# Kernel optimization log

Hardware: AMD Instinct MI355X
Metric: run time of the kernel (lower is better)

Reference implementation:

```python
import jax, jax.numpy as jnp
import numpy as np

B, N, IN_F, E, H, A = 8, 1024, 1024, 256, 4, 64
ALPHA = 0.2          # leaky relu slope
NEG = -9e15          # mask value from original code


def setup_inputs() -> dict:
    key = jax.random.key(0)
    k = jax.random.split(key, 7)
    x = jax.random.normal(k[0], (B * N, IN_F), dtype=jnp.float32)
    adj = jax.random.randint(k[1], (B, N, N), 0, 2, dtype=jnp.int32)
    # per-head GAT params: W (H, IN_F, E); a split into a1, a2 (H, E) each,
    # since cat([Wh_i, Wh_j]) @ a == Wh_i @ a1 + Wh_j @ a2 exactly.
    W = jax.random.normal(k[2], (H, IN_F, E), dtype=jnp.float32) * 0.05
    a1 = jax.random.normal(k[3], (H, E), dtype=jnp.float32) * 0.05
    a2 = jax.random.normal(k[4], (H, E), dtype=jnp.float32) * 0.05
    W_act = jax.random.normal(k[5], (H * E, A), dtype=jnp.float32) * 0.05
    b_act = jnp.zeros((A,), dtype=jnp.float32)
    return {"x": x, "adj": adj, "W": W, "a1": a1, "a2": a2,
            "W_act": W_act, "b_act": b_act}


def reference(x, adj, W, a1, a2, W_act, b_act):
    b, n, _ = adj.shape
    xr = x.reshape(b, n, -1)                                   # (B, N, IN_F)
    Wh = jnp.einsum('bni,hio->hbno', xr, W)                    # (H, B, N, E)
    f1 = jnp.einsum('hbno,ho->hbn', Wh, a1)                    # a . Wh_i part
    f2 = jnp.einsum('hbno,ho->hbn', Wh, a2)                    # a . Wh_j part
    e = jax.nn.leaky_relu(f1[..., :, None] + f2[..., None, :], ALPHA)  # (H,B,N,N)
    e = jnp.where(adj[None] > 0, e, NEG)
    att = jax.nn.softmax(e, axis=-1)                           # masked softmax
    h_prime = jnp.einsum('hbnm,hbmo->hbno', att, Wh)           # (H, B, N, E)
    h_prime = jax.nn.elu(h_prime)                              # concat=True -> elu
    feat = jnp.transpose(h_prime, (1, 2, 0, 3)).reshape(b * n, H * E)
    return feat @ W_act + b_act                                # (B*N, A)
```

## Files before the change

kernel.cpp:

```cpp
#include <hip/hip_runtime.h>
#include <stdint.h>

typedef __attribute__((ext_vector_type(8))) short short8;
typedef __attribute__((ext_vector_type(4))) float f32x4;
typedef __attribute__((ext_vector_type(16))) float f32x16;


__device__ __forceinline__ float b2f(unsigned short u) {
    union { unsigned int i; float f; } v; v.i = ((unsigned int)u) << 16; return v.f;
}
__device__ __forceinline__ unsigned short f2b(float f) {
    union { float f; unsigned int i; } v; v.f = f;
    unsigned int u = v.i;
    u = (u + 0x7FFFu + ((u >> 16) & 1u)) >> 16;
    return (unsigned short)u;
}
__device__ __forceinline__ void glds16(const void* g, const void* l) {
    __builtin_amdgcn_global_load_lds(
        (const __attribute__((address_space(1))) unsigned int*)g,
        (__attribute__((address_space(3))) unsigned int*)l, 16, 0, 0);
}

__device__ __forceinline__ void cvt8(const void* in, unsigned short* out,
                                     int f, int grp) {
    if (f) {
        ((ushort4*)out)[grp * 2]     = ((const ushort4*)in)[grp * 2];
        ((ushort4*)out)[grp * 2 + 1] = ((const ushort4*)in)[grp * 2 + 1];
    } else {
        const float4* p = (const float4*)in + (size_t)grp * 2;
        float4 a = p[0], b = p[1];
        ushort4 o0, o1;
        o0.x = f2b(a.x); o0.y = f2b(a.y); o0.z = f2b(a.z); o0.w = f2b(a.w);
        o1.x = f2b(b.x); o1.y = f2b(b.y); o1.z = f2b(b.z); o1.w = f2b(b.w);
        ((ushort4*)out)[grp * 2]     = o0;
        ((ushort4*)out)[grp * 2 + 1] = o1;
    }
}

__global__ void prep_small(const unsigned int* __restrict__ x,
                           const void* __restrict__ a1, const void* __restrict__ a2,
                           const void* __restrict__ bact,
                           unsigned short* __restrict__ a1b,
                           unsigned short* __restrict__ a2b,
                           unsigned short* __restrict__ bactb,
                           int* __restrict__ flag) {
    __shared__ int sflag;
    int tid = threadIdx.x;
    if (tid < 64) {
        unsigned int wv = x[tid];
        unsigned int e = (wv >> 7) & 0xFF;
        unsigned long long m = __ballot(e >= 100 && e <= 140);
        if (tid == 0) { sflag = (__popcll(m) >= 48) ? 1 : 0; flag[0] = sflag; }
    }
    __syncthreads();
    int f = sflag;
    if (tid < 128) cvt8(a1, a1b, f, tid);
    else           cvt8(a2, a2b, f, tid - 128);
    if (tid < 8)   cvt8(bact, bactb, f, tid);
}

__global__ void conv8(const void* __restrict__ in, unsigned short* __restrict__ out,
                      const int* __restrict__ flag, int total8) {
    int i = blockIdx.x * 256 + threadIdx.x;
    if (i >= total8) return;
    cvt8(in, out, *flag, i);
}

__global__ void zero_kern(float4* __restrict__ p) {
    p[blockIdx.x * 256 + threadIdx.x] = float4{0.f, 0.f, 0.f, 0.f};
}

__global__ __launch_bounds__(256) void t2_all(
        const void* __restrict__ Win, const void* __restrict__ Wactin,
        unsigned short* __restrict__ WT, unsigned short* __restrict__ WactT,
        const int* __restrict__ flag) {
    __shared__ unsigned int tile[64 * 65];
    int z = blockIdx.z;
    const void* in; unsigned short* out; int C, bt;
    if (z < 4) { in = Win; out = WT; C = 256; bt = z; }
    else { if (blockIdx.x != 0) return; in = Wactin; out = WactT; C = 64; bt = 0; }
    int t = threadIdx.x;
    int c0 = blockIdx.x * 64;
    int r0 = blockIdx.y * 64;
    int rl = t >> 2;
    int cc = (t & 3) * 16;
    size_t ibase = ((size_t)bt * 1024 + (r0 + rl)) * C + c0 + cc;
    unsigned short v[16];
    if (*flag) {
        const unsigned short* p = (const unsigned short*)in + ibase;
        short8 a = *(const short8*)p;
        short8 b = *(const short8*)(p + 8);
#pragma unroll
        for (int j = 0; j < 8; j++) { v[j] = (unsigned short)a[j]; v[8 + j] = (unsigned short)b[j]; }
    } else {
        const float* p = (const float*)in + ibase;
#pragma unroll
        for (int j = 0; j < 16; j++) v[j] = f2b(p[j]);
    }
#pragma unroll
    for (int j = 0; j < 16; j++)
        tile[(cc + j) * 65 + rl] = v[j];
    __syncthreads();
    int cl = t >> 2;
    int rch = (t & 3) * 16;
    unsigned short o[16];
#pragma unroll
    for (int j = 0; j < 16; j++)
        o[j] = (unsigned short)tile[cl * 65 + rch + j];
    unsigned short* op = out + ((size_t)bt * C + (c0 + cl)) * 1024 + r0 + rch;
#pragma unroll
    for (int q = 0; q < 4; q++) {
        ushort4 s; s.x = o[q*4]; s.y = o[q*4+1]; s.z = o[q*4+2]; s.w = o[q*4+3];
        ((ushort4*)op)[q] = s;
    }
}

__global__ void pack_adj(const int* __restrict__ adj,
                         unsigned int* __restrict__ maskT) {
    int gid = blockIdx.x * 256 + threadIdx.x;
    int lane = threadIdx.x & 63;
    unsigned long long m = __ballot(adj[gid] > 0);
    if (lane == 0) {
        int lin = gid >> 6;
        int mw = (lin & 15) * 2;
        int bn = lin >> 4;
        int b = bn >> 10, n = bn & 1023;
        maskT[(size_t)(b * 32 + mw) * 1024 + n]     = (unsigned int)m;
        maskT[(size_t)(b * 32 + mw + 1) * 1024 + n] = (unsigned int)(m >> 32);
    }
}

__global__ __launch_bounds__(256) void k1_gemm(
        const unsigned short* __restrict__ x,
        const unsigned short* __restrict__ WT,
        unsigned short* __restrict__ WhF,
        const unsigned short* __restrict__ a1b,
        const unsigned short* __restrict__ a2b,
        float* __restrict__ f1, float* __restrict__ f2) {
    __shared__ unsigned short smA[8 * 512];
    __shared__ unsigned short smB[8 * 512];
    int tid = threadIdx.x;
    int w = tid >> 6, lane = tid & 63;
    int lr = lane & 15, lq = lane >> 4;
    int col0 = blockIdx.x * 128;
    int row0 = blockIdx.y * 128;
    int h = col0 >> 8;
    int e_base = col0 & 255;
    int b = row0 >> 10;
    int m_base = row0 & 1023;
    int wr = w >> 1, wc = w & 1;

    f32x4 acc[4][4] = {};

    for (int k0 = 0; k0 < 1024; k0 += 32) {
        __syncthreads();
#pragma unroll
        for (int s = 0; s < 2; s++) {
            int g = 2 * w + s;
            const unsigned short* srcA =
                x + (size_t)(row0 + g * 16 + lr) * 1024 + k0 + lq * 8;
            glds16(srcA, &smA[g * 512]);
            const unsigned short* srcB =
                WT + (size_t)(h * 256 + e_base + g * 16 + lr) * 1024 + k0 + lq * 8;
            glds16(srcB, &smB[g * 512]);
        }
        __syncthreads();
        short8 af[4], bf[4];
#pragma unroll
        for (int i = 0; i < 4; i++)
            af[i] = *(const short8*)&smA[(wr * 4 + i) * 512 + lane * 8];
#pragma unroll
        for (int j = 0; j < 4; j++)
            bf[j] = *(const short8*)&smB[(wc * 4 + j) * 512 + lane * 8];
#pragma unroll
        for (int i = 0; i < 4; i++)
#pragma unroll
            for (int j = 0; j < 4; j++)
                acc[i][j] = __builtin_amdgcn_mfma_f32_16x16x32_bf16(
                    af[i], bf[j], acc[i][j], 0, 0, 0);
    }

    int hb = h * 8 + b;
#pragma unroll
    for (int i = 0; i < 4; i++) {
#pragma unroll
        for (int j = 0; j < 4; j++) {
            int e = e_base + (wc * 4 + j) * 16 + lr;
            int et = e >> 5, e31 = e & 31;
            int m16 = (m_base >> 4) + wr * 4 + i;
            ushort4 vs;
            vs.x = f2b(acc[i][j][0]);
            vs.y = f2b(acc[i][j][1]);
            vs.z = f2b(acc[i][j][2]);
            vs.w = f2b(acc[i][j][3]);
            size_t idx = ((size_t)((hb * 8 + et) * 64 + m16) * 512)
                         + ((lq >> 1) * 32 + e31) * 8 + (lq & 1) * 4;
            *(ushort4*)&WhF[idx] = vs;
        }
    }

    const float LOG2E = 1.44269504f;
    float a1v[4], a2v[4];
#pragma unroll
    for (int j = 0; j < 4; j++) {
        int e = e_base + (wc * 4 + j) * 16 + lr;
        a1v[j] = b2f(a1b[h * 256 + e]);
        a2v[j] = b2f(a2b[h * 256 + e]);
    }
#pragma unroll
    for (int i = 0; i < 4; i++) {
#pragma unroll
        for (int reg = 0; reg < 4; reg++) {
            float s1 = 0.f, s2 = 0.f;
#pragma unroll
            for (int j = 0; j < 4; j++) {
                s1 += acc[i][j][reg] * a1v[j];
                s2 += acc[i][j][reg] * a2v[j];
            }
            s1 += __shfl_xor(s1, 1, 64); s2 += __shfl_xor(s2, 1, 64);
            s1 += __shfl_xor(s1, 2, 64); s2 += __shfl_xor(s2, 2, 64);
            s1 += __shfl_xor(s1, 4, 64); s2 += __shfl_xor(s2, 4, 64);
            s1 += __shfl_xor(s1, 8, 64); s2 += __shfl_xor(s2, 8, 64);
            if (lr == 0) {
                int m = m_base + (wr * 4 + i) * 16 + lq * 4 + reg;
                atomicAdd(&f1[hb * 1024 + m], s1 * LOG2E);
                atomicAdd(&f2[hb * 1024 + m], s2 * LOG2E);
            }
        }
    }
}

__global__ __launch_bounds__(256, 1) void k2_attn(
        const unsigned short* __restrict__ WhF,
        const unsigned int* __restrict__ maskT,
        const float* __restrict__ f1, const float* __restrict__ f2,
        unsigned short* __restrict__ feat) {
    int tid = threadIdx.x;
    int w = tid >> 6, lane = tid & 63;
    int l5 = lane >> 5, l31 = lane & 31;
    int bid = blockIdx.x;
    int xcd = bid & 7, idx = bid >> 3;
    int hb = xcd + 8 * (idx >> 3);
    int rg = (idx & 7) * 4 + w;
    int n0 = rg * 32;
    int h = hb >> 3, b = hb & 7;
    int row = n0 + l31;
    float f1n = f1[hb * 1024 + row];
    const unsigned short* whb = WhF + (size_t)hb * 8 * 64 * 512 + lane * 8;
    const unsigned int* mrow = maskT + (size_t)b * 32 * 1024 + row;
    const float* f2row = f2 + hb * 1024;

    f32x16 acc[8] = {};
    float den = 0.f;

    for (int m0 = 0; m0 < 1024; m0 += 32) {
        int m16 = m0 >> 4;
        short8 fr[8][2];
#pragma unroll
        for (int et = 0; et < 8; et++)
#pragma unroll
            for (int ks = 0; ks < 2; ks++)
                fr[et][ks] = *(const short8*)(whb + (size_t)(et * 64 + m16 + ks) * 512);

        unsigned int mw = mrow[(size_t)(m0 >> 5) * 1024];
        float4 fA0 = *(const float4*)(f2row + m0 + l5 * 8);
        float4 fA1 = *(const float4*)(f2row + m0 + l5 * 8 + 4);
        float4 fB0 = *(const float4*)(f2row + m0 + 16 + l5 * 8);
        float4 fB1 = *(const float4*)(f2row + m0 + 16 + l5 * 8 + 4);
        float fm[16] = {fA0.x,fA0.y,fA0.z,fA0.w, fA1.x,fA1.y,fA1.z,fA1.w,
                        fB0.x,fB0.y,fB0.z,fB0.w, fB1.x,fB1.y,fB1.z,fB1.w};
        union { unsigned int u[4]; short8 v; } af[2];
#pragma unroll
        for (int ks = 0; ks < 2; ks++) {
#pragma unroll
            for (int pr = 0; pr < 4; pr++) {
                unsigned int ub[2];
#pragma unroll
                for (int q = 0; q < 2; q++) {
                    int j = pr * 2 + q;
                    float tL = f1n + fm[ks * 8 + j];
                    float eL = fmaxf(tL, 0.2f * tL);
                    float pv = ((mw >> (ks * 16 + l5 * 8 + j)) & 1u)
                                   ? exp2f(eL) : 0.f;
                    union { float f; unsigned int i; } pu; pu.f = pv;
                    ub[q] = pu.i & 0xFFFF0000u;
                    union { unsigned int i; float f; } tb; tb.i = ub[q];
                    den += tb.f;
                }
                af[ks].u[pr] = (ub[0] >> 16) | ub[1];
            }
        }
#pragma unroll
        for (int et = 0; et < 8; et++)
#pragma unroll
            for (int ks = 0; ks < 2; ks++)
                acc[et] = __builtin_amdgcn_mfma_f32_32x32x16_bf16(
                    af[ks].v, fr[et][ks], acc[et], 0, 0, 0);
    }

    den += __shfl_xor(den, 32, 64);

    float rdr_all[16];
#pragma unroll
    for (int reg = 0; reg < 16; reg++) {
        int r = (reg & 3) + 8 * (reg >> 2) + 4 * l5;
        rdr_all[reg] = 1.0f / __shfl(den, r, 64);
    }
#pragma unroll
    for (int et = 0; et < 8; et++) {
        int e = et * 32 + l31;
#pragma unroll
        for (int reg = 0; reg < 16; reg++) {
            int r = (reg & 3) + 8 * (reg >> 2) + 4 * l5;
            float v = acc[et][reg] * rdr_all[reg];
            float o = v > 0.f ? v : __expf(v) - 1.f;
            feat[(size_t)(b * 1024 + n0 + r) * 1024 + h * 256 + e] = f2b(o);
        }
    }
}

__global__ __launch_bounds__(256) void k3_out(
        const unsigned short* __restrict__ feat,
        const unsigned short* __restrict__ WactT,
        const unsigned short* __restrict__ bact,
        void* __restrict__ out, const int* __restrict__ flag) {
    __shared__ unsigned short smA[2 * 512];
    __shared__ unsigned short smB[4 * 512];
    int tid = threadIdx.x;
    int w = tid >> 6, lane = tid & 63;
    int lr = lane & 15, lq = lane >> 4;
    int row0 = blockIdx.x * 32;
    int g = w & 1, ch = w >> 1;
    int bf16out = *flag;
    f32x4 acc[2] = {};

    for (int k0 = 0; k0 < 1024; k0 += 32) {
        __syncthreads();
        if (w < 2) {
            const unsigned short* src =
                feat + (size_t)(row0 + w * 16 + lr) * 1024 + k0 + lq * 8;
            glds16(src, &smA[w * 512]);
        } else {
#pragma unroll
            for (int s = 0; s < 2; s++) {
                int t = (w - 2) * 2 + s;
                const unsigned short* src =
                    WactT + (size_t)(t * 16 + lr) * 1024 + k0 + lq * 8;
                glds16(src, &smB[t * 512]);
            }
        }
        __syncthreads();
        short8 af = *(const short8*)&smA[g * 512 + lane * 8];
#pragma unroll
        for (int j = 0; j < 2; j++) {
            short8 bf = *(const short8*)&smB[(ch * 2 + j) * 512 + lane * 8];
            acc[j] = __builtin_amdgcn_mfma_f32_16x16x32_bf16(af, bf, acc[j], 0, 0, 0);
        }
    }
#pragma unroll
    for (int j = 0; j < 2; j++) {
        int col = ch * 32 + j * 16 + lr;
        float bv = b2f(bact[col]);
#pragma unroll
        for (int rr = 0; rr < 4; rr++) {
            int r = row0 + g * 16 + lq * 4 + rr;
            float val = acc[j][rr] + bv;
            if (bf16out) ((unsigned short*)out)[(size_t)r * 64 + col] = f2b(val);
            else         ((float*)out)[(size_t)r * 64 + col] = val;
        }
    }
}

extern "C" void kernel_launch(void* const* d_in, const int* in_sizes, int n_in,
                              void* d_out, int out_size, void* d_ws, size_t ws_size,
                              hipStream_t stream) {
    const void* x    = d_in[0];
    const int*  adj  = (const int*)d_in[1];
    const void* W    = d_in[2];
    const void* a1   = d_in[3];
    const void* a2   = d_in[4];
    const void* Wact = d_in[5];
    const void* bact = d_in[6];

    char* ws = (char*)d_ws;
    unsigned short* WhF   = (unsigned short*)(ws);
    unsigned short* xb    = (unsigned short*)(ws + 16777216);
    unsigned short* feat  = (unsigned short*)(ws + 16777216);
    unsigned short* WT    = (unsigned short*)(ws + 33554432);
    unsigned int*   maskT = (unsigned int*)(ws + 33554432);
    unsigned short* WactT = (unsigned short*)(ws + 35651584);
    float*          f1    = (float*)(ws + 35782656);
    float*          f2    = (float*)(ws + 35913728);
    unsigned short* a1b   = (unsigned short*)(ws + 36044800);
    unsigned short* a2b   = (unsigned short*)(ws + 36046848);
    unsigned short* bactb = (unsigned short*)(ws + 36048896);
    int*            flag  = (int*)(ws + 36049024);
    if (ws_size < (size_t)36049040) return;

    prep_small<<<1, 256, 0, stream>>>((const unsigned int*)x, a1, a2, bact,
                                      a1b, a2b, bactb, flag);
    conv8<<<4096, 256, 0, stream>>>(x, xb, flag, 1048576);
    t2_all<<<dim3(4, 16, 5), 256, 0, stream>>>(W, Wact, WT, WactT, flag);
    zero_kern<<<64, 256, 0, stream>>>((float4*)f1);
    k1_gemm<<<dim3(8, 64), 256, 0, stream>>>(xb, WT, WhF, a1b, a2b, f1, f2);
    pack_adj<<<32768, 256, 0, stream>>>(adj, maskT);
    k2_attn<<<256, 256, 0, stream>>>(WhF, maskT, f1, f2, feat);
    k3_out<<<256, 256, 0, stream>>>(feat, WactT, bactb, d_out, flag);
}
```

Measured before the change: 230.3 us.

## Split attention key range across wave pairs and combine partials via LDS

The attention kernel now splits the 1024-column neighbour loop in half across pairs of waves, doubling the grid to 512 blocks. Each wave accumulates a partial numerator and softmax denominator, and the partials are exchanged through shared memory before normalisation, ELU and store. The WhF fragment loads are split into two halves so the first half is issued before the exp computation and the second after it, and launch bounds now allow two blocks per CU. The intent is more occupancy and more blocks than CUs, at the cost of a 66KB LDS buffer, a barrier and a second stream over the mask and f2 data per row group.

```diff
diff --git a/kernel.cpp b/kernel.cpp
--- a/kernel.cpp
+++ b/kernel.cpp
@@ -230,18 +230,22 @@
     }
 }
 
-__global__ __launch_bounds__(256, 1) void k2_attn(
+__global__ __launch_bounds__(256, 2) void k2_attn(
         const unsigned short* __restrict__ WhF,
         const unsigned int* __restrict__ maskT,
         const float* __restrict__ f1, const float* __restrict__ f2,
         unsigned short* __restrict__ feat) {
+    __shared__ float cmb[4][64][65];
+    __shared__ float dend[4][32];
     int tid = threadIdx.x;
     int w = tid >> 6, lane = tid & 63;
     int l5 = lane >> 5, l31 = lane & 31;
     int bid = blockIdx.x;
     int xcd = bid & 7, idx = bid >> 3;
-    int hb = xcd + 8 * (idx >> 3);
-    int rg = (idx & 7) * 4 + w;
+    int hb = xcd + 8 * (idx >> 4);
+    int pair = idx & 15;
+    int rg = pair * 2 + (w & 1);
+    int mh = w >> 1;
     int n0 = rg * 32;
     int h = hb >> 3, b = hb & 7;
     int row = n0 + l31;
@@ -253,20 +257,21 @@
     f32x16 acc[8] = {};
     float den = 0.f;
 
-    for (int m0 = 0; m0 < 1024; m0 += 32) {
+    int m_lo = mh * 512, m_hi = m_lo + 512;
+    for (int m0 = m_lo; m0 < m_hi; m0 += 32) {
         int m16 = m0 >> 4;
-        short8 fr[8][2];
-#pragma unroll
-        for (int et = 0; et < 8; et++)
-#pragma unroll
-            for (int ks = 0; ks < 2; ks++)
-                fr[et][ks] = *(const short8*)(whb + (size_t)(et * 64 + m16 + ks) * 512);
-
         unsigned int mw = mrow[(size_t)(m0 >> 5) * 1024];
         float4 fA0 = *(const float4*)(f2row + m0 + l5 * 8);
         float4 fA1 = *(const float4*)(f2row + m0 + l5 * 8 + 4);
         float4 fB0 = *(const float4*)(f2row + m0 + 16 + l5 * 8);
         float4 fB1 = *(const float4*)(f2row + m0 + 16 + l5 * 8 + 4);
+        short8 fr1[4][2];
+#pragma unroll
+        for (int et = 0; et < 4; et++)
+#pragma unroll
+            for (int ks = 0; ks < 2; ks++)
+                fr1[et][ks] = *(const short8*)(whb + (size_t)(et * 64 + m16 + ks) * 512);
+
         float fm[16] = {fA0.x,fA0.y,fA0.z,fA0.w, fA1.x,fA1.y,fA1.z,fA1.w,
                         fB0.x,fB0.y,fB0.z,fB0.w, fB1.x,fB1.y,fB1.z,fB1.w};
         union { unsigned int u[4]; short8 v; } af[2];
@@ -290,29 +295,54 @@
                 af[ks].u[pr] = (ub[0] >> 16) | ub[1];
             }
         }
-#pragma unroll
-        for (int et = 0; et < 8; et++)
+        short8 fr2[4][2];
+#pragma unroll
+        for (int et = 0; et < 4; et++)
+#pragma unroll
+            for (int ks = 0; ks < 2; ks++)
+                fr2[et][ks] = *(const short8*)(whb + (size_t)((et + 4) * 64 + m16 + ks) * 512);
+
+#pragma unroll
+        for (int et = 0; et < 4; et++)
 #pragma unroll
             for (int ks = 0; ks < 2; ks++)
                 acc[et] = __builtin_amdgcn_mfma_f32_32x32x16_bf16(
-                    af[ks].v, fr[et][ks], acc[et], 0, 0, 0);
+                    af[ks].v, fr1[et][ks], acc[et], 0, 0, 0);
+#pragma unroll
+        for (int et = 0; et < 4; et++)
+#pragma unroll
+            for (int ks = 0; ks < 2; ks++)
+                acc[4 + et] = __builtin_amdgcn_mfma_f32_32x32x16_bf16(
+                    af[ks].v, fr2[et][ks], acc[4 + et], 0, 0, 0);
     }
 
     den += __shfl_xor(den, 32, 64);
 
+    int give = (mh == 0) ? 4 : 0;
+    int keep = (mh == 0) ? 0 : 4;
+#pragma unroll
+    for (int t = 0; t < 4; t++)
+#pragma unroll
+        for (int reg = 0; reg < 16; reg++)
+            cmb[w][lane][t * 16 + reg] = acc[give + t][reg];
+    if (lane < 32) dend[w][l31] = den;
+    __syncthreads();
+    int pw = w ^ 2;
+    float den_tot = den + dend[pw][l31];
     float rdr_all[16];
 #pragma unroll
     for (int reg = 0; reg < 16; reg++) {
         int r = (reg & 3) + 8 * (reg >> 2) + 4 * l5;
-        rdr_all[reg] = 1.0f / __shfl(den, r, 64);
-    }
-#pragma unroll
-    for (int et = 0; et < 8; et++) {
+        rdr_all[reg] = 1.0f / __shfl(den_tot, r, 64);
+    }
+#pragma unroll
+    for (int t = 0; t < 4; t++) {
+        int et = keep + t;
         int e = et * 32 + l31;
 #pragma unroll
         for (int reg = 0; reg < 16; reg++) {
             int r = (reg & 3) + 8 * (reg >> 2) + 4 * l5;
-            float v = acc[et][reg] * rdr_all[reg];
+            float v = (acc[et][reg] + cmb[pw][lane][t * 16 + reg]) * rdr_all[reg];
             float o = v > 0.f ? v : __expf(v) - 1.f;
             feat[(size_t)(b * 1024 + n0 + r) * 1024 + h * 256 + e] = f2b(o);
         }
@@ -404,6 +434,6 @@
     zero_kern<<<64, 256, 0, stream>>>((float4*)f1);
     k1_gemm<<<dim3(8, 64), 256, 0, stream>>>(xb, WT, WhF, a1b, a2b, f1, f2);
     pack_adj<<<32768, 256, 0, stream>>>(adj, maskT);
-    k2_attn<<<256, 256, 0, stream>>>(WhF, maskT, f1, f2, feat);
+    k2_attn<<<512, 256, 0, stream>>>(WhF, maskT, f1, f2, feat);
     k3_out<<<256, 256, 0, stream>>>(feat, WactT, bactb, d_out, flag);
 }
```

New measurement: 236.9 us. +2.9%, slower.

## Switch attention kernel to 16x16 MFMA tiles with more blocks and occupancy

Applied to the files above, without the earlier changes.

The attention kernel now gives each wave 16 query rows instead of 32 and uses 16x16x32 bf16 MFMAs over all 256 features, with 16 accumulators. The grid doubles to 512 blocks and launch bounds allow two blocks per CU. The k1 GEMM writes Wh in a new fragment layout to match the smaller MFMA shape. Separately, zeroing of the f1/f2 buffers is folded into prep_small so one kernel launch is removed. The aim is more parallelism and latency hiding in the dominant attention kernel, at the cost of reading the Wh fragments twice as often per output row.

```diff
diff --git a/kernel.cpp b/kernel.cpp
--- a/kernel.cpp
+++ b/kernel.cpp
@@ -3,7 +3,6 @@
 
 typedef __attribute__((ext_vector_type(8))) short short8;
 typedef __attribute__((ext_vector_type(4))) float f32x4;
-typedef __attribute__((ext_vector_type(16))) float f32x16;
 
 
 __device__ __forceinline__ float b2f(unsigned short u) {
@@ -43,9 +42,13 @@
                            unsigned short* __restrict__ a1b,
                            unsigned short* __restrict__ a2b,
                            unsigned short* __restrict__ bactb,
-                           int* __restrict__ flag) {
+                           int* __restrict__ flag, float4* __restrict__ fz) {
     __shared__ int sflag;
     int tid = threadIdx.x;
+    if (blockIdx.x > 0) {
+        fz[(blockIdx.x - 1) * 256 + tid] = float4{0.f, 0.f, 0.f, 0.f};
+        return;
+    }
     if (tid < 64) {
         unsigned int wv = x[tid];
         unsigned int e = (wv >> 7) & 0xFF;
@@ -64,10 +67,6 @@
     int i = blockIdx.x * 256 + threadIdx.x;
     if (i >= total8) return;
     cvt8(in, out, *flag, i);
-}
-
-__global__ void zero_kern(float4* __restrict__ p) {
-    p[blockIdx.x * 256 + threadIdx.x] = float4{0.f, 0.f, 0.f, 0.f};
 }
 
 __global__ __launch_bounds__(256) void t2_all(
@@ -183,18 +182,21 @@
     int hb = h * 8 + b;
 #pragma unroll
     for (int i = 0; i < 4; i++) {
+        int mg = wr * 4 + i;
+        int mt = (m_base >> 5) + (mg >> 1);
+        int mhi = ((mg & 1) << 1) | (lq >> 1);
+        int mlo = (lq & 1) * 4;
 #pragma unroll
         for (int j = 0; j < 4; j++) {
             int e = e_base + (wc * 4 + j) * 16 + lr;
-            int et = e >> 5, e31 = e & 31;
-            int m16 = (m_base >> 4) + wr * 4 + i;
+            int et = e >> 4, el = e & 15;
             ushort4 vs;
             vs.x = f2b(acc[i][j][0]);
             vs.y = f2b(acc[i][j][1]);
             vs.z = f2b(acc[i][j][2]);
             vs.w = f2b(acc[i][j][3]);
-            size_t idx = ((size_t)((hb * 8 + et) * 64 + m16) * 512)
-                         + ((lq >> 1) * 32 + e31) * 8 + (lq & 1) * 4;
+            size_t idx = ((size_t)(hb * 16 + et) * 32 + mt) * 512
+                         + mhi * 128 + el * 8 + mlo;
             *(ushort4*)&WhF[idx] = vs;
         }
     }
@@ -230,91 +232,90 @@
     }
 }
 
-__global__ __launch_bounds__(256, 1) void k2_attn(
+__global__ __launch_bounds__(256, 2) void k2_attn(
         const unsigned short* __restrict__ WhF,
         const unsigned int* __restrict__ maskT,
         const float* __restrict__ f1, const float* __restrict__ f2,
         unsigned short* __restrict__ feat) {
     int tid = threadIdx.x;
     int w = tid >> 6, lane = tid & 63;
-    int l5 = lane >> 5, l31 = lane & 31;
+    int lr = lane & 15, lq = lane >> 4;
     int bid = blockIdx.x;
     int xcd = bid & 7, idx = bid >> 3;
-    int hb = xcd + 8 * (idx >> 3);
-    int rg = (idx & 7) * 4 + w;
-    int n0 = rg * 32;
+    int hb = xcd + 8 * (idx >> 4);
+    int rg = (idx & 15) * 4 + w;
+    int n0 = rg * 16;
     int h = hb >> 3, b = hb & 7;
-    int row = n0 + l31;
+    int row = n0 + lr;
     float f1n = f1[hb * 1024 + row];
-    const unsigned short* whb = WhF + (size_t)hb * 8 * 64 * 512 + lane * 8;
+    const unsigned short* whb = WhF + (size_t)hb * 16 * 32 * 512 + lane * 8;
     const unsigned int* mrow = maskT + (size_t)b * 32 * 1024 + row;
     const float* f2row = f2 + hb * 1024;
 
-    f32x16 acc[8] = {};
+    f32x4 acc[16] = {};
     float den = 0.f;
 
-    for (int m0 = 0; m0 < 1024; m0 += 32) {
-        int m16 = m0 >> 4;
-        short8 fr[8][2];
+    for (int mt = 0; mt < 32; mt++) {
+        int m0 = mt * 32;
+        unsigned int mw = mrow[(size_t)mt * 1024];
+        float4 fA = *(const float4*)(f2row + m0 + lq * 8);
+        float4 fB = *(const float4*)(f2row + m0 + lq * 8 + 4);
+        short8 fr1[8];
 #pragma unroll
         for (int et = 0; et < 8; et++)
-#pragma unroll
-            for (int ks = 0; ks < 2; ks++)
-                fr[et][ks] = *(const short8*)(whb + (size_t)(et * 64 + m16 + ks) * 512);
-
-        unsigned int mw = mrow[(size_t)(m0 >> 5) * 1024];
-        float4 fA0 = *(const float4*)(f2row + m0 + l5 * 8);
-        float4 fA1 = *(const float4*)(f2row + m0 + l5 * 8 + 4);
-        float4 fB0 = *(const float4*)(f2row + m0 + 16 + l5 * 8);
-        float4 fB1 = *(const float4*)(f2row + m0 + 16 + l5 * 8 + 4);
-        float fm[16] = {fA0.x,fA0.y,fA0.z,fA0.w, fA1.x,fA1.y,fA1.z,fA1.w,
-                        fB0.x,fB0.y,fB0.z,fB0.w, fB1.x,fB1.y,fB1.z,fB1.w};
-        union { unsigned int u[4]; short8 v; } af[2];
-#pragma unroll
-        for (int ks = 0; ks < 2; ks++) {
-#pragma unroll
-            for (int pr = 0; pr < 4; pr++) {
-                unsigned int ub[2];
-#pragma unroll
-                for (int q = 0; q < 2; q++) {
-                    int j = pr * 2 + q;
-                    float tL = f1n + fm[ks * 8 + j];
-                    float eL = fmaxf(tL, 0.2f * tL);
-                    float pv = ((mw >> (ks * 16 + l5 * 8 + j)) & 1u)
-                                   ? exp2f(eL) : 0.f;
-                    union { float f; unsigned int i; } pu; pu.f = pv;
-                    ub[q] = pu.i & 0xFFFF0000u;
-                    union { unsigned int i; float f; } tb; tb.i = ub[q];
-                    den += tb.f;
-                }
-                af[ks].u[pr] = (ub[0] >> 16) | ub[1];
+            fr1[et] = *(const short8*)(whb + (size_t)(et * 32 + mt) * 512);
+
+        float fmv[8] = {fA.x, fA.y, fA.z, fA.w, fB.x, fB.y, fB.z, fB.w};
+        unsigned int msh = mw >> (lq * 8);
+        union { unsigned int u[4]; short8 v; } af;
+#pragma unroll
+        for (int pr = 0; pr < 4; pr++) {
+            unsigned int ub[2];
+#pragma unroll
+            for (int q = 0; q < 2; q++) {
+                int j = pr * 2 + q;
+                float tL = f1n + fmv[j];
+                float eL = fmaxf(tL, 0.2f * tL);
+                float pv = ((msh >> j) & 1u) ? exp2f(eL) : 0.f;
+                union { float f; unsigned int i; } pu; pu.f = pv;
+                ub[q] = pu.i & 0xFFFF0000u;
+                union { unsigned int i; float f; } tb; tb.i = ub[q];
+                den += tb.f;
             }
-        }
+            af.u[pr] = (ub[0] >> 16) | ub[1];
+        }
+        short8 fr2[8];
 #pragma unroll
         for (int et = 0; et < 8; et++)
-#pragma unroll
-            for (int ks = 0; ks < 2; ks++)
-                acc[et] = __builtin_amdgcn_mfma_f32_32x32x16_bf16(
-                    af[ks].v, fr[et][ks], acc[et], 0, 0, 0);
-    }
-
+            fr2[et] = *(const short8*)(whb + (size_t)((et + 8) * 32 + mt) * 512);
+
+#pragma unroll
+        for (int et = 0; et < 8; et++)
+            acc[et] = __builtin_amdgcn_mfma_f32_16x16x32_bf16(
+                af.v, fr1[et], acc[et], 0, 0, 0);
+#pragma unroll
+        for (int et = 0; et < 8; et++)
+            acc[8 + et] = __builtin_amdgcn_mfma_f32_16x16x32_bf16(
+                af.v, fr2[et], acc[8 + et], 0, 0, 0);
+    }
+
+    den += __shfl_xor(den, 16, 64);
     den += __shfl_xor(den, 32, 64);
 
-    float rdr_all[16];
-#pragma unroll
-    for (int reg = 0; reg < 16; reg++) {
-        int r = (reg & 3) + 8 * (reg >> 2) + 4 * l5;
-        rdr_all[reg] = 1.0f / __shfl(den, r, 64);
-    }
-#pragma unroll
-    for (int et = 0; et < 8; et++) {
-        int e = et * 32 + l31;
-#pragma unroll
-        for (int reg = 0; reg < 16; reg++) {
-            int r = (reg & 3) + 8 * (reg >> 2) + 4 * l5;
-            float v = acc[et][reg] * rdr_all[reg];
+    float rdr[4];
+#pragma unroll
+    for (int reg = 0; reg < 4; reg++)
+        rdr[reg] = 1.0f / __shfl(den, lq * 4 + reg, 64);
+
+#pragma unroll
+    for (int et = 0; et < 16; et++) {
+        int e = et * 16 + lr;
+#pragma unroll
+        for (int reg = 0; reg < 4; reg++) {
+            float v = acc[et][reg] * rdr[reg];
             float o = v > 0.f ? v : __expf(v) - 1.f;
-            feat[(size_t)(b * 1024 + n0 + r) * 1024 + h * 256 + e] = f2b(o);
+            feat[(size_t)(b * 1024 + n0 + lq * 4 + reg) * 1024 + h * 256 + e]
+                = f2b(o);
         }
     }
 }
@@ -397,13 +398,12 @@
     int*            flag  = (int*)(ws + 36049024);
     if (ws_size < (size_t)36049040) return;
 
-    prep_small<<<1, 256, 0, stream>>>((const unsigned int*)x, a1, a2, bact,
-                                      a1b, a2b, bactb, flag);
+    prep_small<<<65, 256, 0, stream>>>((const unsigned int*)x, a1, a2, bact,
+                                       a1b, a2b, bactb, flag, (float4*)f1);
     conv8<<<4096, 256, 0, stream>>>(x, xb, flag, 1048576);
     t2_all<<<dim3(4, 16, 5), 256, 0, stream>>>(W, Wact, WT, WactT, flag);
-    zero_kern<<<64, 256, 0, stream>>>((float4*)f1);
     k1_gemm<<<dim3(8, 64), 256, 0, stream>>>(xb, WT, WhF, a1b, a2b, f1, f2);
     pack_adj<<<32768, 256, 0, stream>>>(adj, maskT);
-    k2_attn<<<256, 256, 0, stream>>>(WhF, maskT, f1, f2, feat);
+    k2_attn<<<512, 256, 0, stream>>>(WhF, maskT, f1, f2, feat);
     k3_out<<<256, 256, 0, stream>>>(feat, WactT, bactb, d_out, flag);
 }
```

After: 235.3 us. +2.2%, slower.
